# Optimization experiments

Hardware: AMD Instinct MI355X
Metric: run time of the kernel (lower is better)

Reference implementation:

```python
import jax, jax.numpy as jnp
import numpy as np

N = 50000      # nodes
E = 800000     # edges
H = 128        # hidden_features
EF = 8         # edge_features (before distance concat)
L = 2          # num_layers
NF = 100.0     # normalization_factor
NC = 1.0       # norm_constant
ATTN = True
USE_TANH = False
TANH_RANGE = 15.0
EIN = 2 * H + EF + 1  # GCL / coord-MLP edge input dim


def setup_inputs() -> dict:
    key = jax.random.key(0)
    ks = jax.random.split(key, 16)
    s = 0.02
    w = lambda k, shape: (jax.random.normal(k, shape, jnp.float32) * s)
    return dict(
        x=jax.random.normal(ks[0], (N, H), jnp.float32),
        pos=jax.random.normal(ks[1], (N, 3), jnp.float32),
        mask=jnp.ones((N, 1), jnp.float32),
        edge_attr=jax.random.normal(ks[2], (E, EF), jnp.float32),
        edge_index=jax.random.randint(ks[3], (2, E), 0, N),
        # GCL layer params, stacked over L layers
        W_e1=w(ks[4], (L, EIN, H)), b_e1=jnp.zeros((L, H), jnp.float32),
        W_e2=w(ks[5], (L, H, H)),  b_e2=jnp.zeros((L, H), jnp.float32),
        W_att=w(ks[6], (L, H, 1)), b_att=jnp.zeros((L, 1), jnp.float32),
        W_n1=w(ks[7], (L, 2 * H, H)), b_n1=jnp.zeros((L, H), jnp.float32),
        W_n2=w(ks[8], (L, H, H)),  b_n2=jnp.zeros((L, H), jnp.float32),
        # Equivariant coordinate-update MLP (last layer has no bias)
        cW1=w(ks[9], (EIN, H)), cb1=jnp.zeros((H,), jnp.float32),
        cW2=w(ks[10], (H, H)), cb2=jnp.zeros((H,), jnp.float32),
        cW3=w(ks[11], (H, 1)),
    )


def reference(x, pos, mask, edge_attr, edge_index,
              W_e1, b_e1, W_e2, b_e2, W_att, b_att, W_n1, b_n1, W_n2, b_n2,
              cW1, cb1, cW2, cb2, cW3):
    silu = jax.nn.silu
    row, col = edge_index[0], edge_index[1]  # aggregate messages at row
    diff = pos[row] - pos[col]                         # [E, 3]
    d2 = jnp.sum(diff * diff, axis=-1, keepdims=True)  # [E, 1] squared distance
    ea = jnp.concatenate([d2, edge_attr], axis=-1)     # [E, EF+1]

    # GCL message-passing layers (residual node update)
    for l in range(L):
        he = jnp.concatenate([x[row], x[col], ea], axis=-1)   # [E, EIN]
        m = silu(silu(he @ W_e1[l] + b_e1[l]) @ W_e2[l] + b_e2[l])
        if ATTN:
            m = m * jax.nn.sigmoid(m @ W_att[l] + b_att[l])
        agg = jax.ops.segment_sum(m, row, num_segments=N) / NF
        x = x + silu(jnp.concatenate([x, agg], axis=-1) @ W_n1[l] + b_n1[l]) @ W_n2[l] + b_n2[l]

    # Equivariant coordinate update
    he = jnp.concatenate([x[row], x[col], ea], axis=-1)
    phi = silu(silu(he @ cW1 + cb1) @ cW2 + cb2) @ cW3        # [E, 1]
    if USE_TANH:
        phi = jnp.tanh(phi) * TANH_RANGE
    nd = diff / (jnp.sqrt(d2) + NC)                           # normalized direction
    trans = nd * phi                                          # [E, 3]
    pos = pos + (jax.ops.segment_sum(trans, row, num_segments=N) / NF) * mask
    return (x, pos)
```

## Files before the change

kernel.cpp:

```cpp
#include <hip/hip_runtime.h>
#include <hip/hip_bf16.h>
#include <stdint.h>

#define NN 50000
#define NE 800000
#define HH 128

typedef __bf16 bf16x8 __attribute__((ext_vector_type(8)));
typedef float  f32x4  __attribute__((ext_vector_type(4)));
typedef long   f8frag;

__device__ __forceinline__ unsigned short f2bf(float f) {
  union { float f; uint32_t u; } v; v.f = f;
  uint32_t r = v.u + 0x7FFFu + ((v.u >> 16) & 1u);
  return (unsigned short)(r >> 16);
}
__device__ __forceinline__ float b2f(unsigned short u) {
  union { float f; uint32_t u; } v; v.u = (uint32_t)u << 16; return v.f;
}
#if __has_builtin(__builtin_amdgcn_cvt_pk_bf16_f32)
typedef __bf16 bf16x2 __attribute__((ext_vector_type(2)));
__device__ __forceinline__ uint32_t pack2bf(float a, float b) {
  union { bf16x2 v; uint32_t u; } t;
  t.v = __builtin_amdgcn_cvt_pk_bf16_f32(a, b);
  return t.u;
}
#else
__device__ __forceinline__ uint32_t pack2bf(float a, float b) {
  return (uint32_t)f2bf(a) | ((uint32_t)f2bf(b) << 16);
}
#endif
__device__ __forceinline__ uint8_t f2fp8(float v) {
  return (uint8_t)(__builtin_amdgcn_cvt_pk_fp8_f32(v, 0.f, 0, false) & 0xff);
}
__device__ __forceinline__ float silu_f(float x) {
  return x * __builtin_amdgcn_rcpf(1.f + __expf(-x));
}
__device__ __forceinline__ float sigm_f(float x) {
  return __builtin_amdgcn_rcpf(1.f + __expf(-x));
}

__device__ __forceinline__ bf16x8 frag_ld(const short* blk, int row, int q) {
  int c = q ^ ((row >> 1) & 3);
  return *(const bf16x8*)(blk + row * 32 + c * 8);
}
__device__ __forceinline__ int wfrag_off(int row, int q) {
  return row * 32 + ((q ^ ((row >> 1) & 3)) * 8);
}

__global__ void k_prep_weights(const float* We1, const float* We2, const float* Wn1,
                               const float* Wn2, const float* cW1, const float* cW2,
                               uint8_t* W1f8, short* W2sw, short* Wn1sw, short* Wn2sw,
                               short* W1csw) {
  int idx = blockIdx.x * 256 + threadIdx.x;
  if (idx < 110592) {
    int l = idx / 36864, rem = idx % 36864;
    const float* s = (l == 0) ? We1 : (l == 1) ? We1 + 33920 : cW1;
    int kkb = rem >> 12, r2 = rem & 4095;
    int n = r2 >> 5, kw = r2 & 31;
    int k = kkb * 32 + kw;
    float v = (k < 265) ? s[k * 128 + n] : 0.f;
    W1f8[idx] = f2fp8(v);
    return;
  }
  idx -= 110592;
  if (idx < 49152) {
    int l = idx >> 14, rem = idx & 16383;
    const float* s = (l == 0) ? We2 : (l == 1) ? We2 + 16384 : cW2;
    int kkb = rem >> 12, r2 = rem & 4095, n = r2 >> 5, kw = r2 & 31;
    int cp = kw >> 3, j = kw & 7, c = cp ^ ((n >> 1) & 3);
    int k = kkb * 32 + c * 8 + j;
    W2sw[(l << 14) + (rem)] = (short)f2bf(s[k * 128 + n]);
    return;
  }
  idx -= 49152;
  if (idx < 65536) {
    int l = idx >> 15, rem = idx & 32767;
    const float* s = Wn1 + l * 32768;
    int kkb = rem >> 12, r2 = rem & 4095, n = r2 >> 5, kw = r2 & 31;
    int cp = kw >> 3, j = kw & 7, c = cp ^ ((n >> 1) & 3);
    int k = kkb * 32 + c * 8 + j;
    Wn1sw[(l << 15) + rem] = (short)f2bf(s[k * 128 + n]);
    return;
  }
  idx -= 65536;
  if (idx < 32768) {
    int l = idx >> 14, rem = idx & 16383;
    const float* s = Wn2 + l * 16384;
    int kkb = rem >> 12, r2 = rem & 4095, n = r2 >> 5, kw = r2 & 31;
    int cp = kw >> 3, j = kw & 7, c = cp ^ ((n >> 1) & 3);
    int k = kkb * 32 + c * 8 + j;
    Wn2sw[(l << 14) + rem] = (short)f2bf(s[k * 128 + n]);
    return;
  }
  idx -= 32768;
  if (idx < 98304) {
    int l = idx / 32768, rem = idx % 32768;
    const float* s = (l == 0) ? We1 : (l == 1) ? We1 + 33920 : cW1;
    int kkb = rem >> 13, r2 = rem & 8191, n = r2 >> 5, kw = r2 & 31;
    int cp = kw >> 3, j = kw & 7, c = cp ^ ((n >> 1) & 3);
    int k = kkb * 32 + c * 8 + j;
    float v = (n < 128) ? s[k * 128 + n] : s[(128 + k) * 128 + (n - 128)];
    W1csw[l * 32768 + rem] = (short)f2bf(v);
  }
}

__global__ void k_x_prep(const float* __restrict__ x, short* __restrict__ Anode) {
  int i = blockIdx.x * 256 + threadIdx.x;
  if (i < NN * 32) {
    float4 v = ((const float4*)x)[i];
    int node = i >> 5, c4 = (i & 31) << 2;
    ushort4 pk;
    pk.x = f2bf(v.x); pk.y = f2bf(v.y); pk.z = f2bf(v.z); pk.w = f2bf(v.w);
    *(ushort4*)(Anode + node * 256 + c4) = pk;
  }
}
__global__ void k_nodeprep(const float* __restrict__ agg, short* __restrict__ Anode) {
  int i = blockIdx.x * 256 + threadIdx.x;
  if (i < NN * HH) Anode[(i >> 7) * 256 + 128 + (i & 127)] = (short)f2bf(agg[i] * 0.01f);
}
__global__ void k_edge_pre(const float* __restrict__ pos, const float* __restrict__ eattr,
                           const int* __restrict__ ei, const int* __restrict__ inv,
                           int* __restrict__ rowS, int* __restrict__ colS,
                           uint8_t* __restrict__ eaF8, float* __restrict__ ndS) {
  int e = blockIdx.x * 256 + threadIdx.x;
  if (e >= NE) return;
  int r = ei[e], c = ei[NE + e];
  float dx = pos[r * 3 + 0] - pos[c * 3 + 0];
  float dy = pos[r * 3 + 1] - pos[c * 3 + 1];
  float dz = pos[r * 3 + 2] - pos[c * 3 + 2];
  float d2 = dx * dx + dy * dy + dz * dz;
  float invd = __builtin_amdgcn_rcpf(sqrtf(d2) + 1.f);
  int p = inv[e];
  rowS[p] = r;
  colS[p] = c;
  ndS[p * 3 + 0] = dx * invd;
  ndS[p * 3 + 1] = dy * invd;
  ndS[p * 3 + 2] = dz * invd;
  const float* ea = eattr + (size_t)e * 8;
  uint32_t w0 = __builtin_amdgcn_cvt_pk_fp8_f32(d2, ea[0], 0, false);
  w0 = __builtin_amdgcn_cvt_pk_fp8_f32(ea[1], ea[2], w0, true);
  uint32_t w1 = __builtin_amdgcn_cvt_pk_fp8_f32(ea[3], ea[4], 0, false);
  w1 = __builtin_amdgcn_cvt_pk_fp8_f32(ea[5], ea[6], w1, true);
  uint32_t w2 = __builtin_amdgcn_cvt_pk_fp8_f32(ea[7], 0.f, 0, false);
  uint4 v = {w0, w1, w2, 0u};
  *(uint4*)(eaF8 + (size_t)p * 16) = v;
}
__global__ void k_pos_final(const float* __restrict__ pos, const float* __restrict__ mask,
                            const float* __restrict__ pagg, float* __restrict__ out) {
  int i = blockIdx.x * 256 + threadIdx.x;
  if (i < NN * 3) out[i] = pos[i] + pagg[i] * 0.01f * mask[i / 3];
}

__global__ void k_hist(const int* __restrict__ ei, int* __restrict__ cnt) {
  int e = blockIdx.x * 256 + threadIdx.x;
  if (e < NE) atomicAdd(&cnt[ei[e]], 1);
}
__global__ void k_scan_block(const int* __restrict__ cnt, int* __restrict__ offs,
                             int* __restrict__ bsum) {
  __shared__ int s[256];
  int i = blockIdx.x * 256 + threadIdx.x;
  int v = (i < NN) ? cnt[i] : 0;
  s[threadIdx.x] = v;
  __syncthreads();
#pragma unroll
  for (int d = 1; d < 256; d <<= 1) {
    int t = (threadIdx.x >= d) ? s[threadIdx.x - d] : 0;
    __syncthreads();
    s[threadIdx.x] += t;
    __syncthreads();
  }
  if (i < NN) offs[i] = s[threadIdx.x] - v;
  if (threadIdx.x == 255) bsum[blockIdx.x] = s[255];
}
__global__ void k_scan_top(int* __restrict__ bsum) {
  __shared__ int s[256];
  int v = (threadIdx.x < 196) ? bsum[threadIdx.x] : 0;
  s[threadIdx.x] = v;
  __syncthreads();
#pragma unroll
  for (int d = 1; d < 256; d <<= 1) {
    int t = (threadIdx.x >= d) ? s[threadIdx.x - d] : 0;
    __syncthreads();
    s[threadIdx.x] += t;
    __syncthreads();
  }
  if (threadIdx.x < 196) bsum[threadIdx.x] = s[threadIdx.x] - v;
}
__global__ void k_scan_add(int* __restrict__ offs, const int* __restrict__ bsum) {
  int i = blockIdx.x * 256 + threadIdx.x;
  if (i < NN) offs[i] += bsum[blockIdx.x];
}
__global__ void k_scatter(const int* __restrict__ ei, int* __restrict__ offs,
                          int* __restrict__ inv) {
  int e = blockIdx.x * 256 + threadIdx.x;
  if (e < NE) inv[e] = atomicAdd(&offs[ei[e]], 1);
}

__global__ __launch_bounds__(256) void k_h1(
    const short* __restrict__ Anode, const short* __restrict__ W1c,
    const float* __restrict__ b1, short* __restrict__ H1RC) {
  const int tid = threadIdx.x, lane = tid & 63, w = tid >> 6;
  const int ln = lane & 15, q = lane >> 4;
  const int tile = blockIdx.x;
  size_t nbase[4];
  int wofs[4];
#pragma unroll
  for (int i = 0; i < 4; ++i) {
    int node = tile * 64 + i * 16 + ln;
    nbase[i] = (size_t)(node < NN ? node : (NN - 1)) * 256;
    int row = w * 64 + i * 16 + ln;
    wofs[i] = row * 32 + ((q ^ ((row >> 1) & 3)) * 8);
  }
  f32x4 acc[4][4];
  const f32x4 zero4 = {0.f, 0.f, 0.f, 0.f};
#pragma unroll
  for (int mi = 0; mi < 4; ++mi)
#pragma unroll
    for (int ni = 0; ni < 4; ++ni) acc[mi][ni] = zero4;
#pragma unroll
  for (int kk = 0; kk < 4; ++kk) {
    bf16x8 af[4], bfr[4];
#pragma unroll
    for (int i = 0; i < 4; ++i) af[i] = *(const bf16x8*)(Anode + nbase[i] + kk * 32 + q * 8);
#pragma unroll
    for (int i = 0; i < 4; ++i) bfr[i] = *(const bf16x8*)(W1c + kk * 8192 + wofs[i]);
#pragma unroll
    for (int mi = 0; mi < 4; ++mi)
#pragma unroll
      for (int ni = 0; ni < 4; ++ni)
        acc[mi][ni] = __builtin_amdgcn_mfma_f32_16x16x32_bf16(af[mi], bfr[ni], acc[mi][ni], 0, 0, 0);
  }
  float b1v[4];
#pragma unroll
  for (int ni = 0; ni < 4; ++ni) {
    int ch = w * 64 + ni * 16 + ln;
    b1v[ni] = (ch < 128) ? b1[ch] : 0.f;
  }
#pragma unroll
  for (int mi = 0; mi < 4; ++mi)
#pragma unroll
    for (int r = 0; r < 4; ++r) {
      int node = tile * 64 + mi * 16 + q * 4 + r;
      if (node < NN) {
#pragma unroll
        for (int ni = 0; ni < 4; ++ni) {
          int ch = w * 64 + ni * 16 + ln;
          H1RC[(size_t)node * 256 + ch] = (short)f2bf(acc[mi][ni][r] + b1v[ni]);
        }
      }
    }
}

template <int COORD>
__global__ __launch_bounds__(256, 4) void k_edge_gemm(
    const short* __restrict__ H1RC, const uint8_t* __restrict__ eaF8,
    const int* __restrict__ rowS, const int* __restrict__ colS,
    const uint8_t* __restrict__ W1f8, const short* __restrict__ W2l,
    const float* __restrict__ b2,
    const float* __restrict__ wred, const float* __restrict__ batt,
    const float* __restrict__ ndS, float* outAcc) {
  __shared__ __align__(16) short A2s[8192];
  __shared__ float redp[64][2];
  __shared__ float redv[64];
  __shared__ int srow[64];
  __shared__ __align__(8) unsigned char srunS[64];
  __shared__ int runrowS[64];
  __shared__ int cntS[1];

  const int tid = threadIdx.x;
  const int lane = tid & 63;
  const int w = tid >> 6;
  const int ln = lane & 15, q = lane >> 4;
  const int wm = w >> 1, wn = w & 1;
  const int tile = blockIdx.x;

  if (tid < 64) srow[tid] = rowS[tile * 64 + tid];
  __syncthreads();

  bool is_start = (tid < 64) && (tid == 0 || srow[tid] != srow[tid - 1]);
  unsigned long long bmask = __ballot(is_start);
  if (tid == 0) cntS[0] = __popcll(bmask);
  if (tid < 64) {
    int run = __popcll(bmask & ((1ull << lane) - 1ull)) + (is_start ? 1 : 0) - 1;
    srunS[tid] = (unsigned char)run;
    if (is_start) runrowS[run] = srow[tid];
  }

  const int e0 = wm * 32 + ln, e1 = e0 + 16;
  const size_t hr0 = (size_t)srow[e0] * 256, hr1 = (size_t)srow[e1] * 256;
  const size_t hc0 = (size_t)colS[tile * 64 + e0] * 256 + 128;
  const size_t hc1 = (size_t)colS[tile * 64 + e1] * 256 + 128;
  const size_t ea0 = (size_t)(tile * 64 + e0) * 16 + (q & 1) * 8;
  const size_t ea1 = (size_t)(tile * 64 + e1) * 16 + (q & 1) * 8;
  int wofs8[4], wofs[4];
#pragma unroll
  for (int i = 0; i < 4; ++i) {
    wofs8[i] = (wn * 64 + i * 16 + ln) * 32 + q * 8;
    wofs[i] = wfrag_off(wn * 64 + i * 16 + ln, q);
  }

  ushort4 xr[4][2], xc[4][2];
#pragma unroll
  for (int ni = 0; ni < 4; ++ni) {
    int cb = wn * 64 + ni * 16 + q * 4;
    xr[ni][0] = *(const ushort4*)(H1RC + hr0 + cb);
    xr[ni][1] = *(const ushort4*)(H1RC + hr1 + cb);
    xc[ni][0] = *(const ushort4*)(H1RC + hc0 + cb);
    xc[ni][1] = *(const ushort4*)(H1RC + hc1 + cb);
  }

  f32x4 acc[4][2];
  const f32x4 zero4 = {0.f, 0.f, 0.f, 0.f};
#pragma unroll
  for (int ni = 0; ni < 4; ++ni)
#pragma unroll
    for (int mi = 0; mi < 2; ++mi) acc[ni][mi] = zero4;

  {
    const uint8_t* W1ea = W1f8 + 8 * 4096;
    f8frag wf[4], hf[2];
#pragma unroll
    for (int i = 0; i < 4; ++i) wf[i] = *(const f8frag*)(W1ea + wofs8[i]);
    hf[0] = (q < 2) ? *(const f8frag*)(eaF8 + ea0) : 0L;
    hf[1] = (q < 2) ? *(const f8frag*)(eaF8 + ea1) : 0L;
#pragma unroll
    for (int ni = 0; ni < 4; ++ni)
#pragma unroll
      for (int mi = 0; mi < 2; ++mi)
        acc[ni][mi] = __builtin_amdgcn_mfma_f32_16x16x32_fp8_fp8(wf[ni], hf[mi], acc[ni][mi], 0, 0, 0);
  }

#pragma unroll
  for (int ni = 0; ni < 4; ++ni) {
    int cb = wn * 64 + ni * 16 + q * 4;
    int kkb = cb >> 5, cc = (cb >> 3) & 3, j0 = cb & 7;
#pragma unroll
    for (int mi = 0; mi < 2; ++mi) {
      int edge = wm * 32 + mi * 16 + ln;
      int addr = kkb * 2048 + edge * 32 + ((cc ^ ((edge >> 1) & 3)) * 8) + j0;
      float h0 = silu_f(acc[ni][mi][0] + b2f(xr[ni][mi].x) + b2f(xc[ni][mi].x));
      float h1 = silu_f(acc[ni][mi][1] + b2f(xr[ni][mi].y) + b2f(xc[ni][mi].y));
      float h2 = silu_f(acc[ni][mi][2] + b2f(xr[ni][mi].z) + b2f(xc[ni][mi].z));
      float h3 = silu_f(acc[ni][mi][3] + b2f(xr[ni][mi].w) + b2f(xc[ni][mi].w));
      uint2 pk;
      pk.x = pack2bf(h0, h1);
      pk.y = pack2bf(h2, h3);
      *(uint2*)(A2s + addr) = pk;
    }
  }
  __syncthreads();

  f32x4 acc2[4][2];
#pragma unroll
  for (int ni = 0; ni < 4; ++ni)
#pragma unroll
    for (int mi = 0; mi < 2; ++mi) acc2[ni][mi] = zero4;
#pragma unroll
  for (int kk = 0; kk < 4; ++kk) {
    bf16x8 wf[4], hf[2];
#pragma unroll
    for (int i = 0; i < 4; ++i) wf[i] = *(const bf16x8*)(W2l + kk * 4096 + wofs[i]);
#pragma unroll
    for (int i = 0; i < 2; ++i) hf[i] = frag_ld(A2s + kk * 2048, wm * 32 + i * 16 + ln, q);
#pragma unroll
    for (int ni = 0; ni < 4; ++ni)
#pragma unroll
      for (int mi = 0; mi < 2; ++mi)
        acc2[ni][mi] = __builtin_amdgcn_mfma_f32_16x16x32_bf16(wf[ni], hf[mi], acc2[ni][mi], 0, 0, 0);
  }

  float4 b2v[4], wv[4];
#pragma unroll
  for (int ni = 0; ni < 4; ++ni) {
    b2v[ni] = *(const float4*)(b2 + wn * 64 + ni * 16 + q * 4);
    wv[ni]  = *(const float4*)(wred + wn * 64 + ni * 16 + q * 4);
  }
  float p[2] = {0.f, 0.f};
#pragma unroll
  for (int ni = 0; ni < 4; ++ni)
#pragma unroll
    for (int mi = 0; mi < 2; ++mi)
#pragma unroll
      for (int r = 0; r < 4; ++r) {
        float v = silu_f(acc2[ni][mi][r] + ((const float*)&b2v[ni])[r]);
        acc2[ni][mi][r] = v;
        p[mi] += v * ((const float*)&wv[ni])[r];
      }
#pragma unroll
  for (int mi = 0; mi < 2; ++mi) {
    p[mi] += __shfl_xor(p[mi], 16, 64);
    p[mi] += __shfl_xor(p[mi], 32, 64);
  }
  if (lane < 16) {
#pragma unroll
    for (int mi = 0; mi < 2; ++mi) redp[wm * 32 + mi * 16 + ln][wn] = p[mi];
  }
  __syncthreads();

  if (COORD == 0) {
    if (tid < 64) redv[tid] = sigm_f(redp[tid][0] + redp[tid][1] + batt[0]);
    __syncthreads();
    float attv[2] = {redv[wm * 32 + ln], redv[wm * 32 + 16 + ln]};
#pragma unroll
    for (int ni = 0; ni < 4; ++ni)
#pragma unroll
      for (int mi = 0; mi < 2; ++mi) {
        int eb = mi * 16 + ln;
        int cE = (eb >> 3) & 3, jE = eb & 7;
#pragma unroll
        for (int r = 0; r < 4; ++r) {
          int chan2 = wn * 64 + ni * 16 + q * 4 + r;
          int addr = wm * 4096 + chan2 * 32 + ((cE ^ ((chan2 >> 1) & 3)) * 8) + jE;
          union { float f; uint32_t u; } vv;
          vv.f = acc2[ni][mi][r] * attv[mi];
          A2s[addr] = (short)((vv.u + 0x8000u) >> 16);
        }
      }
    __syncthreads();
    const int nruns = cntS[0];
    bf16x8 bfrg[2][2];
#pragma unroll
    for (int kk = 0; kk < 2; ++kk)
#pragma unroll
      for (int ni = 0; ni < 2; ++ni)
        bfrg[kk][ni] = frag_ld(A2s + kk * 4096, w * 32 + ni * 16 + ln, q);
    const int npass = (nruns + 15) >> 4;
    for (int pp = 0; pp < npass; ++pp) {
      const unsigned int base = pp * 16;
      f32x4 a3c[2] = {zero4, zero4};
#pragma unroll
      for (int kk = 0; kk < 2; ++kk) {
        uint2 sb = *(const uint2*)(srunS + kk * 32 + q * 8);
        union { short s[8]; bf16x8 v; } af;
#pragma unroll
        for (int j = 0; j < 4; ++j)
          af.s[j] = (((sb.x >> (8 * j)) & 255u) == base + (unsigned)ln) ? (short)0x3F80 : (short)0;
#pragma unroll
        for (int j = 0; j < 4; ++j)
          af.s[4 + j] = (((sb.y >> (8 * j)) & 255u) == base + (unsigned)ln) ? (short)0x3F80 : (short)0;
        a3c[0] = __builtin_amdgcn_mfma_f32_16x16x32_bf16(af.v, bfrg[kk][0], a3c[0], 0, 0, 0);
        a3c[1] = __builtin_amdgcn_mfma_f32_16x16x32_bf16(af.v, bfrg[kk][1], a3c[1], 0, 0, 0);
      }
#pragma unroll
      for (int ni = 0; ni < 2; ++ni)
#pragma unroll
        for (int r = 0; r < 4; ++r) {
          int run = (int)base + q * 4 + r;
          if (run < nruns) {
            int rw = runrowS[run];
            atomicAdd(&outAcc[(size_t)rw * 128 + (w * 32 + ni * 16 + ln)], a3c[ni][r]);
          }
        }
    }
  } else {
    float* ndl = (float*)A2s;
    if (tid < 64) {
      float phi = redp[tid][0] + redp[tid][1];
      ndl[tid * 3 + 0] = ndS[(size_t)(tile * 64 + tid) * 3 + 0] * phi;
      ndl[tid * 3 + 1] = ndS[(size_t)(tile * 64 + tid) * 3 + 1] * phi;
      ndl[tid * 3 + 2] = ndS[(size_t)(tile * 64 + tid) * 3 + 2] * phi;
    }
    __syncthreads();
    if (is_start) {
      int myrow = srow[tid];
      float s0 = 0.f, s1 = 0.f, s2 = 0.f;
      for (int j = tid; j < 64 && srow[j] == myrow; ++j) {
        s0 += ndl[j * 3 + 0];
        s1 += ndl[j * 3 + 1];
        s2 += ndl[j * 3 + 2];
      }
      atomicAdd(&outAcc[myrow * 3 + 0], s0);
      atomicAdd(&outAcc[myrow * 3 + 1], s1);
      atomicAdd(&outAcc[myrow * 3 + 2], s2);
    }
  }
}

__global__ __launch_bounds__(256) void k_node_gemm(
    short* Anode, const short* __restrict__ Wn1l, const short* __restrict__ Wn2l,
    const float* __restrict__ b1, const float* __restrict__ b2,
    const float* __restrict__ xres, float* __restrict__ xout) {
  __shared__ short A2s[4 * 4096];

  const int tid = threadIdx.x;
  const int lane = tid & 63;
  const int w = tid >> 6;
  const int ln = lane & 15, q = lane >> 4;
  const int wm = w >> 1, wn = w & 1;
  const int tile = blockIdx.x;

  size_t nbase[4];
  int wofs[4];
#pragma unroll
  for (int i = 0; i < 4; ++i) {
    int node = tile * 128 + wm * 64 + i * 16 + ln;
    nbase[i] = (size_t)(node < NN ? node : (NN - 1)) * 256;
    wofs[i] = wfrag_off(wn * 64 + i * 16 + ln, q);
  }

  f32x4 acc[4][4];
  const f32x4 zero4 = {0.f, 0.f, 0.f, 0.f};
#pragma unroll
  for (int mi = 0; mi < 4; ++mi)
#pragma unroll
    for (int ni = 0; ni < 4; ++ni) acc[mi][ni] = zero4;

#pragma unroll
  for (int kk = 0; kk < 8; ++kk) {
    bf16x8 af[4], bfr[4];
#pragma unroll
    for (int i = 0; i < 4; ++i) af[i] = *(const bf16x8*)(Anode + nbase[i] + kk * 32 + q * 8);
#pragma unroll
    for (int i = 0; i < 4; ++i) bfr[i] = *(const bf16x8*)(Wn1l + kk * 4096 + wofs[i]);
#pragma unroll
    for (int mi = 0; mi < 4; ++mi)
#pragma unroll
      for (int ni = 0; ni < 4; ++ni)
        acc[mi][ni] = __builtin_amdgcn_mfma_f32_16x16x32_bf16(af[mi], bfr[ni], acc[mi][ni], 0, 0, 0);
  }

  float b1v[4];
#pragma unroll
  for (int ni = 0; ni < 4; ++ni) b1v[ni] = b1[wn * 64 + ni * 16 + ln];
#pragma unroll
  for (int mi = 0; mi < 4; ++mi)
#pragma unroll
    for (int ni = 0; ni < 4; ++ni) {
      int chan = wn * 64 + ni * 16 + ln;
      int kkb = chan >> 5, c = (chan >> 3) & 3, jj = chan & 7;
#pragma unroll
      for (int r = 0; r < 4; ++r) {
        int m = wm * 64 + mi * 16 + q * 4 + r;
        float v = silu_f(acc[mi][ni][r] + b1v[ni]);
        A2s[kkb * 4096 + m * 32 + ((c ^ ((m >> 1) & 3)) * 8) + jj] = (short)f2bf(v);
      }
    }
  __syncthreads();

  f32x4 acc2[4][4];
#pragma unroll
  for (int mi = 0; mi < 4; ++mi)
#pragma unroll
    for (int ni = 0; ni < 4; ++ni) acc2[mi][ni] = zero4;
#pragma unroll
  for (int kk = 0; kk < 4; ++kk) {
    bf16x8 af[4], bfr[4];
#pragma unroll
    for (int i = 0; i < 4; ++i) af[i] = frag_ld(A2s + kk * 4096, wm * 64 + i * 16 + ln, q);
#pragma unroll
    for (int i = 0; i < 4; ++i) bfr[i] = *(const bf16x8*)(Wn2l + kk * 4096 + wofs[i]);
#pragma unroll
    for (int mi = 0; mi < 4; ++mi)
#pragma unroll
      for (int ni = 0; ni < 4; ++ni)
        acc2[mi][ni] = __builtin_amdgcn_mfma_f32_16x16x32_bf16(af[mi], bfr[ni], acc2[mi][ni], 0, 0, 0);
  }

  float b2v[4];
#pragma unroll
  for (int ni = 0; ni < 4; ++ni) b2v[ni] = b2[wn * 64 + ni * 16 + ln];
#pragma unroll
  for (int mi = 0; mi < 4; ++mi)
#pragma unroll
    for (int r = 0; r < 4; ++r) {
      int m = wm * 64 + mi * 16 + q * 4 + r;
      int node = tile * 128 + m;
      if (node < NN) {
#pragma unroll
        for (int ni = 0; ni < 4; ++ni) {
          int chan = wn * 64 + ni * 16 + ln;
          float v = acc2[mi][ni][r] + b2v[ni] + xres[(size_t)node * 128 + chan];
          xout[(size_t)node * 128 + chan] = v;
          Anode[(size_t)node * 256 + chan] = (short)f2bf(v);
        }
      }
    }
}

extern "C" void kernel_launch(void* const* d_in, const int* in_sizes, int n_in,
                              void* d_out, int out_size, void* d_ws, size_t ws_size,
                              hipStream_t stream) {
  const float* x    = (const float*)d_in[0];
  const float* pos  = (const float*)d_in[1];
  const float* mask = (const float*)d_in[2];
  const float* eattr= (const float*)d_in[3];
  const int*   ei   = (const int*)d_in[4];
  const float* We1  = (const float*)d_in[5];
  const float* be1  = (const float*)d_in[6];
  const float* We2  = (const float*)d_in[7];
  const float* be2  = (const float*)d_in[8];
  const float* Watt = (const float*)d_in[9];
  const float* batt = (const float*)d_in[10];
  const float* Wn1  = (const float*)d_in[11];
  const float* bn1  = (const float*)d_in[12];
  const float* Wn2  = (const float*)d_in[13];
  const float* bn2  = (const float*)d_in[14];
  const float* cW1  = (const float*)d_in[15];
  const float* cb1  = (const float*)d_in[16];
  const float* cW2  = (const float*)d_in[17];
  const float* cb2  = (const float*)d_in[18];
  const float* cW3  = (const float*)d_in[19];

  char* p = (char*)d_ws;
  auto carve = [&](size_t bytes) { char* r = p; p += (bytes + 511) & ~(size_t)511; return r; };
  short*   Anode = (short*)carve((size_t)NN * 256 * 2);
  short*   H1RC  = (short*)carve((size_t)NN * 256 * 2);
  uint8_t* eaF8  = (uint8_t*)carve((size_t)NE * 16 + 256);
  int*     rowS  = (int*)carve((size_t)NE * 4);
  int*     colS  = (int*)carve((size_t)NE * 4);
  float*   ndS   = (float*)carve((size_t)NE * 3 * 4);
  float*   agg   = (float*)carve((size_t)NN * 128 * 4);
  float*   xcur  = (float*)carve((size_t)NN * 128 * 4);
  float*   pagg  = (float*)carve((size_t)NN * 3 * 4);
  uint8_t* W1f8  = (uint8_t*)carve(3 * 36864);
  short*   W2sw  = (short*)carve(3 * 16384 * 2);
  short*   Wn1sw = (short*)carve(2 * 32768 * 2);
  short*   Wn2sw = (short*)carve(2 * 16384 * 2);
  short*   W1csw = (short*)carve(3 * 32768 * 2);
  int*     cnt   = (int*)carve((size_t)NN * 4);
  int*     offs  = (int*)carve((size_t)NN * 4);
  int*     bsum  = (int*)carve(256 * 4);
  int*     inv   = (int*)carve((size_t)NE * 4);

  float* xout_f = (float*)d_out;
  float* pout_f = xout_f + NN * 128;

  k_prep_weights<<<1392, 256, 0, stream>>>(We1, We2, Wn1, Wn2, cW1, cW2,
                                           W1f8, W2sw, Wn1sw, Wn2sw, W1csw);
  k_x_prep<<<6250, 256, 0, stream>>>(x, Anode);

  hipMemsetAsync(cnt, 0, (size_t)NN * 4, stream);
  k_hist<<<3125, 256, 0, stream>>>(ei, cnt);
  k_scan_block<<<196, 256, 0, stream>>>(cnt, offs, bsum);
  k_scan_top<<<1, 256, 0, stream>>>(bsum);
  k_scan_add<<<196, 256, 0, stream>>>(offs, bsum);
  k_scatter<<<3125, 256, 0, stream>>>(ei, offs, inv);
  k_edge_pre<<<3125, 256, 0, stream>>>(pos, eattr, ei, inv, rowS, colS, eaF8, ndS);

  for (int l = 0; l < 2; ++l) {
    k_h1<<<782, 256, 0, stream>>>(Anode, W1csw + l * 32768, be1 + l * 128, H1RC);
    hipMemsetAsync(agg, 0, (size_t)NN * 128 * 4, stream);
    k_edge_gemm<0><<<12500, 256, 0, stream>>>(H1RC, eaF8, rowS, colS,
        W1f8 + l * 36864, W2sw + l * 16384, be2 + l * 128,
        Watt + l * 128, batt + l, (const float*)nullptr, agg);
    k_nodeprep<<<25000, 256, 0, stream>>>(agg, Anode);
    k_node_gemm<<<391, 256, 0, stream>>>(Anode,
        Wn1sw + l * 32768, Wn2sw + l * 16384, bn1 + l * 128, bn2 + l * 128,
        l == 0 ? x : xcur, l == 0 ? xcur : xout_f);
  }
  k_h1<<<782, 256, 0, stream>>>(Anode, W1csw + 2 * 32768, cb1, H1RC);
  hipMemsetAsync(pagg, 0, (size_t)NN * 3 * 4, stream);
  k_edge_gemm<1><<<12500, 256, 0, stream>>>(H1RC, eaF8, rowS, colS,
      W1f8 + 2 * 36864, W2sw + 2 * 16384, cb2, cW3, (const float*)nullptr, ndS, pagg);
  k_pos_final<<<587, 256, 0, stream>>>(pos, mask, pagg, pout_f);
}
```

Baseline: 799.8 us.

## Fuse agg conversion into node GEMM, permute H1RC layout, fold attention into scatter

Removes the separate k_nodeprep kernel: the node GEMM now reads fp32 agg directly, scales and packs it to bf16 in-register, and Anode shrinks to 128 channels per node. k_h1 writes H1RC in a permuted channel order so the edge GEMM can gather row/col features with two 16-byte loads per edge instead of four 8-byte loads, using 32-bit offsets. The attention sigmoid is stored as bf16 and applied as the weight in the one-hot segment-reduction MFMA, which drops a sync and a multiply per element. The node GEMM tile is halved to 64 nodes, doubling the grid size to raise occupancy.

```diff
diff --git a/kernel.cpp b/kernel.cpp
--- a/kernel.cpp
+++ b/kernel.cpp
@@ -109,15 +109,10 @@
   int i = blockIdx.x * 256 + threadIdx.x;
   if (i < NN * 32) {
     float4 v = ((const float4*)x)[i];
-    int node = i >> 5, c4 = (i & 31) << 2;
     ushort4 pk;
     pk.x = f2bf(v.x); pk.y = f2bf(v.y); pk.z = f2bf(v.z); pk.w = f2bf(v.w);
-    *(ushort4*)(Anode + node * 256 + c4) = pk;
-  }
-}
-__global__ void k_nodeprep(const float* __restrict__ agg, short* __restrict__ Anode) {
-  int i = blockIdx.x * 256 + threadIdx.x;
-  if (i < NN * HH) Anode[(i >> 7) * 256 + 128 + (i & 127)] = (short)f2bf(agg[i] * 0.01f);
+    *(ushort4*)(Anode + i * 4) = pk;
+  }
 }
 __global__ void k_edge_pre(const float* __restrict__ pos, const float* __restrict__ eattr,
                            const int* __restrict__ ei, const int* __restrict__ inv,
@@ -208,7 +203,7 @@
 #pragma unroll
   for (int i = 0; i < 4; ++i) {
     int node = tile * 64 + i * 16 + ln;
-    nbase[i] = (size_t)(node < NN ? node : (NN - 1)) * 256;
+    nbase[i] = (size_t)(node < NN ? node : (NN - 1)) * 128;
     int row = w * 64 + i * 16 + ln;
     wofs[i] = row * 32 + ((q ^ ((row >> 1) & 3)) * 8);
   }
@@ -245,8 +240,8 @@
       if (node < NN) {
 #pragma unroll
         for (int ni = 0; ni < 4; ++ni) {
-          int ch = w * 64 + ni * 16 + ln;
-          H1RC[(size_t)node * 256 + ch] = (short)f2bf(acc[mi][ni][r] + b1v[ni]);
+          int ph = (w >> 1) * 128 + (w & 1) * 64 + ((ln >> 2) << 4) + (ni << 2) + (ln & 3);
+          H1RC[(size_t)node * 256 + ph] = (short)f2bf(acc[mi][ni][r] + b1v[ni]);
         }
       }
     }
@@ -262,7 +257,7 @@
     const float* __restrict__ ndS, float* outAcc) {
   __shared__ __align__(16) short A2s[8192];
   __shared__ float redp[64][2];
-  __shared__ float redv[64];
+  __shared__ __align__(16) unsigned short attb[64];
   __shared__ int srow[64];
   __shared__ __align__(8) unsigned char srunS[64];
   __shared__ int runrowS[64];
@@ -288,11 +283,13 @@
   }
 
   const int e0 = wm * 32 + ln, e1 = e0 + 16;
-  const size_t hr0 = (size_t)srow[e0] * 256, hr1 = (size_t)srow[e1] * 256;
-  const size_t hc0 = (size_t)colS[tile * 64 + e0] * 256 + 128;
-  const size_t hc1 = (size_t)colS[tile * 64 + e1] * 256 + 128;
-  const size_t ea0 = (size_t)(tile * 64 + e0) * 16 + (q & 1) * 8;
-  const size_t ea1 = (size_t)(tile * 64 + e1) * 16 + (q & 1) * 8;
+  const uint32_t cbp = (uint32_t)(wn * 64 + q * 16);
+  const uint32_t hr0 = (uint32_t)srow[e0] * 256u + cbp;
+  const uint32_t hr1 = (uint32_t)srow[e1] * 256u + cbp;
+  const uint32_t hc0 = (uint32_t)colS[tile * 64 + e0] * 256u + 128u + cbp;
+  const uint32_t hc1 = (uint32_t)colS[tile * 64 + e1] * 256u + 128u + cbp;
+  const uint32_t ea0 = (uint32_t)(tile * 64 + e0) * 16u + (uint32_t)((q & 1) * 8);
+  const uint32_t ea1 = (uint32_t)(tile * 64 + e1) * 16u + (uint32_t)((q & 1) * 8);
   int wofs8[4], wofs[4];
 #pragma unroll
   for (int i = 0; i < 4; ++i) {
@@ -300,15 +297,16 @@
     wofs[i] = wfrag_off(wn * 64 + i * 16 + ln, q);
   }
 
-  ushort4 xr[4][2], xc[4][2];
-#pragma unroll
-  for (int ni = 0; ni < 4; ++ni) {
-    int cb = wn * 64 + ni * 16 + q * 4;
-    xr[ni][0] = *(const ushort4*)(H1RC + hr0 + cb);
-    xr[ni][1] = *(const ushort4*)(H1RC + hr1 + cb);
-    xc[ni][0] = *(const ushort4*)(H1RC + hc0 + cb);
-    xc[ni][1] = *(const ushort4*)(H1RC + hc1 + cb);
-  }
+  union U8 { uint4 v; unsigned short s[8]; };
+  U8 xr[2][2], xc[2][2];
+  xr[0][0].v = *(const uint4*)(H1RC + hr0);
+  xr[0][1].v = *(const uint4*)(H1RC + hr0 + 8);
+  xr[1][0].v = *(const uint4*)(H1RC + hr1);
+  xr[1][1].v = *(const uint4*)(H1RC + hr1 + 8);
+  xc[0][0].v = *(const uint4*)(H1RC + hc0);
+  xc[0][1].v = *(const uint4*)(H1RC + hc0 + 8);
+  xc[1][0].v = *(const uint4*)(H1RC + hc1);
+  xc[1][1].v = *(const uint4*)(H1RC + hc1 + 8);
 
   f32x4 acc[4][2];
   const f32x4 zero4 = {0.f, 0.f, 0.f, 0.f};
@@ -335,14 +333,15 @@
   for (int ni = 0; ni < 4; ++ni) {
     int cb = wn * 64 + ni * 16 + q * 4;
     int kkb = cb >> 5, cc = (cb >> 3) & 3, j0 = cb & 7;
+    const int hh = ni >> 1, b4 = (ni & 1) * 4;
 #pragma unroll
     for (int mi = 0; mi < 2; ++mi) {
       int edge = wm * 32 + mi * 16 + ln;
       int addr = kkb * 2048 + edge * 32 + ((cc ^ ((edge >> 1) & 3)) * 8) + j0;
-      float h0 = silu_f(acc[ni][mi][0] + b2f(xr[ni][mi].x) + b2f(xc[ni][mi].x));
-      float h1 = silu_f(acc[ni][mi][1] + b2f(xr[ni][mi].y) + b2f(xc[ni][mi].y));
-      float h2 = silu_f(acc[ni][mi][2] + b2f(xr[ni][mi].z) + b2f(xc[ni][mi].z));
-      float h3 = silu_f(acc[ni][mi][3] + b2f(xr[ni][mi].w) + b2f(xc[ni][mi].w));
+      float h0 = silu_f(acc[ni][mi][0] + b2f(xr[mi][hh].s[b4 + 0]) + b2f(xc[mi][hh].s[b4 + 0]));
+      float h1 = silu_f(acc[ni][mi][1] + b2f(xr[mi][hh].s[b4 + 1]) + b2f(xc[mi][hh].s[b4 + 1]));
+      float h2 = silu_f(acc[ni][mi][2] + b2f(xr[mi][hh].s[b4 + 2]) + b2f(xc[mi][hh].s[b4 + 2]));
+      float h3 = silu_f(acc[ni][mi][3] + b2f(xr[mi][hh].s[b4 + 3]) + b2f(xc[mi][hh].s[b4 + 3]));
       uint2 pk;
       pk.x = pack2bf(h0, h1);
       pk.y = pack2bf(h2, h3);
@@ -399,9 +398,7 @@
   __syncthreads();
 
   if (COORD == 0) {
-    if (tid < 64) redv[tid] = sigm_f(redp[tid][0] + redp[tid][1] + batt[0]);
-    __syncthreads();
-    float attv[2] = {redv[wm * 32 + ln], redv[wm * 32 + 16 + ln]};
+    if (tid < 64) attb[tid] = f2bf(sigm_f(redp[tid][0] + redp[tid][1] + batt[0]));
 #pragma unroll
     for (int ni = 0; ni < 4; ++ni)
 #pragma unroll
@@ -413,7 +410,7 @@
           int chan2 = wn * 64 + ni * 16 + q * 4 + r;
           int addr = wm * 4096 + chan2 * 32 + ((cE ^ ((chan2 >> 1) & 3)) * 8) + jE;
           union { float f; uint32_t u; } vv;
-          vv.f = acc2[ni][mi][r] * attv[mi];
+          vv.f = acc2[ni][mi][r];
           A2s[addr] = (short)((vv.u + 0x8000u) >> 16);
         }
       }
@@ -432,13 +429,15 @@
 #pragma unroll
       for (int kk = 0; kk < 2; ++kk) {
         uint2 sb = *(const uint2*)(srunS + kk * 32 + q * 8);
+        U8 ab;
+        ab.v = *(const uint4*)(attb + kk * 32 + q * 8);
         union { short s[8]; bf16x8 v; } af;
 #pragma unroll
         for (int j = 0; j < 4; ++j)
-          af.s[j] = (((sb.x >> (8 * j)) & 255u) == base + (unsigned)ln) ? (short)0x3F80 : (short)0;
+          af.s[j] = (((sb.x >> (8 * j)) & 255u) == base + (unsigned)ln) ? (short)ab.s[j] : (short)0;
 #pragma unroll
         for (int j = 0; j < 4; ++j)
-          af.s[4 + j] = (((sb.y >> (8 * j)) & 255u) == base + (unsigned)ln) ? (short)0x3F80 : (short)0;
+          af.s[4 + j] = (((sb.y >> (8 * j)) & 255u) == base + (unsigned)ln) ? (short)ab.s[4 + j] : (short)0;
         a3c[0] = __builtin_amdgcn_mfma_f32_16x16x32_bf16(af.v, bfrg[kk][0], a3c[0], 0, 0, 0);
         a3c[1] = __builtin_amdgcn_mfma_f32_16x16x32_bf16(af.v, bfrg[kk][1], a3c[1], 0, 0, 0);
       }
@@ -478,10 +477,11 @@
 }
 
 __global__ __launch_bounds__(256) void k_node_gemm(
-    short* Anode, const short* __restrict__ Wn1l, const short* __restrict__ Wn2l,
+    short* Anode, const float* __restrict__ agg,
+    const short* __restrict__ Wn1l, const short* __restrict__ Wn2l,
     const float* __restrict__ b1, const float* __restrict__ b2,
     const float* __restrict__ xres, float* __restrict__ xout) {
-  __shared__ short A2s[4 * 4096];
+  __shared__ short A2s[4 * 2048];
 
   const int tid = threadIdx.x;
   const int lane = tid & 63;
@@ -490,31 +490,48 @@
   const int wm = w >> 1, wn = w & 1;
   const int tile = blockIdx.x;
 
-  size_t nbase[4];
+  int nidx[2];
+  size_t nbase[2];
   int wofs[4];
 #pragma unroll
-  for (int i = 0; i < 4; ++i) {
-    int node = tile * 128 + wm * 64 + i * 16 + ln;
-    nbase[i] = (size_t)(node < NN ? node : (NN - 1)) * 256;
-    wofs[i] = wfrag_off(wn * 64 + i * 16 + ln, q);
-  }
-
-  f32x4 acc[4][4];
+  for (int i = 0; i < 2; ++i) {
+    int node = tile * 64 + wm * 32 + i * 16 + ln;
+    nidx[i] = node < NN ? node : (NN - 1);
+    nbase[i] = (size_t)nidx[i] * 128;
+  }
+#pragma unroll
+  for (int i = 0; i < 4; ++i) wofs[i] = wfrag_off(wn * 64 + i * 16 + ln, q);
+
+  f32x4 acc[2][4];
   const f32x4 zero4 = {0.f, 0.f, 0.f, 0.f};
 #pragma unroll
-  for (int mi = 0; mi < 4; ++mi)
+  for (int mi = 0; mi < 2; ++mi)
 #pragma unroll
     for (int ni = 0; ni < 4; ++ni) acc[mi][ni] = zero4;
 
 #pragma unroll
   for (int kk = 0; kk < 8; ++kk) {
-    bf16x8 af[4], bfr[4];
-#pragma unroll
-    for (int i = 0; i < 4; ++i) af[i] = *(const bf16x8*)(Anode + nbase[i] + kk * 32 + q * 8);
+    bf16x8 af[2], bfr[4];
+#pragma unroll
+    for (int i = 0; i < 2; ++i) {
+      if (kk < 4) {
+        af[i] = *(const bf16x8*)(Anode + nbase[i] + kk * 32 + q * 8);
+      } else {
+        const float* ag = agg + nbase[i] + (kk - 4) * 32 + q * 8;
+        float4 lo = *(const float4*)ag;
+        float4 hi = *(const float4*)(ag + 4);
+        union { uint32_t u[4]; bf16x8 v; } t;
+        t.u[0] = pack2bf(lo.x * 0.01f, lo.y * 0.01f);
+        t.u[1] = pack2bf(lo.z * 0.01f, lo.w * 0.01f);
+        t.u[2] = pack2bf(hi.x * 0.01f, hi.y * 0.01f);
+        t.u[3] = pack2bf(hi.z * 0.01f, hi.w * 0.01f);
+        af[i] = t.v;
+      }
+    }
 #pragma unroll
     for (int i = 0; i < 4; ++i) bfr[i] = *(const bf16x8*)(Wn1l + kk * 4096 + wofs[i]);
 #pragma unroll
-    for (int mi = 0; mi < 4; ++mi)
+    for (int mi = 0; mi < 2; ++mi)
 #pragma unroll
       for (int ni = 0; ni < 4; ++ni)
         acc[mi][ni] = __builtin_amdgcn_mfma_f32_16x16x32_bf16(af[mi], bfr[ni], acc[mi][ni], 0, 0, 0);
@@ -524,34 +541,34 @@
 #pragma unroll
   for (int ni = 0; ni < 4; ++ni) b1v[ni] = b1[wn * 64 + ni * 16 + ln];
 #pragma unroll
-  for (int mi = 0; mi < 4; ++mi)
+  for (int mi = 0; mi < 2; ++mi)
 #pragma unroll
     for (int ni = 0; ni < 4; ++ni) {
       int chan = wn * 64 + ni * 16 + ln;
       int kkb = chan >> 5, c = (chan >> 3) & 3, jj = chan & 7;
 #pragma unroll
       for (int r = 0; r < 4; ++r) {
-        int m = wm * 64 + mi * 16 + q * 4 + r;
+        int m = wm * 32 + mi * 16 + q * 4 + r;
         float v = silu_f(acc[mi][ni][r] + b1v[ni]);
-        A2s[kkb * 4096 + m * 32 + ((c ^ ((m >> 1) & 3)) * 8) + jj] = (short)f2bf(v);
+        A2s[kkb * 2048 + m * 32 + ((c ^ ((m >> 1) & 3)) * 8) + jj] = (short)f2bf(v);
       }
     }
   __syncthreads();
 
-  f32x4 acc2[4][4];
-#pragma unroll
-  for (int mi = 0; mi < 4; ++mi)
+  f32x4 acc2[2][4];
+#pragma unroll
+  for (int mi = 0; mi < 2; ++mi)
 #pragma unroll
     for (int ni = 0; ni < 4; ++ni) acc2[mi][ni] = zero4;
 #pragma unroll
   for (int kk = 0; kk < 4; ++kk) {
-    bf16x8 af[4], bfr[4];
-#pragma unroll
-    for (int i = 0; i < 4; ++i) af[i] = frag_ld(A2s + kk * 4096, wm * 64 + i * 16 + ln, q);
+    bf16x8 af[2], bfr[4];
+#pragma unroll
+    for (int i = 0; i < 2; ++i) af[i] = frag_ld(A2s + kk * 2048, wm * 32 + i * 16 + ln, q);
 #pragma unroll
     for (int i = 0; i < 4; ++i) bfr[i] = *(const bf16x8*)(Wn2l + kk * 4096 + wofs[i]);
 #pragma unroll
-    for (int mi = 0; mi < 4; ++mi)
+    for (int mi = 0; mi < 2; ++mi)
 #pragma unroll
       for (int ni = 0; ni < 4; ++ni)
         acc2[mi][ni] = __builtin_amdgcn_mfma_f32_16x16x32_bf16(af[mi], bfr[ni], acc2[mi][ni], 0, 0, 0);
@@ -561,18 +578,18 @@
 #pragma unroll
   for (int ni = 0; ni < 4; ++ni) b2v[ni] = b2[wn * 64 + ni * 16 + ln];
 #pragma unroll
-  for (int mi = 0; mi < 4; ++mi)
+  for (int mi = 0; mi < 2; ++mi)
 #pragma unroll
     for (int r = 0; r < 4; ++r) {
-      int m = wm * 64 + mi * 16 + q * 4 + r;
-      int node = tile * 128 + m;
+      int m = wm * 32 + mi * 16 + q * 4 + r;
+      int node = tile * 64 + m;
       if (node < NN) {
 #pragma unroll
         for (int ni = 0; ni < 4; ++ni) {
           int chan = wn * 64 + ni * 16 + ln;
           float v = acc2[mi][ni][r] + b2v[ni] + xres[(size_t)node * 128 + chan];
           xout[(size_t)node * 128 + chan] = v;
-          Anode[(size_t)node * 256 + chan] = (short)f2bf(v);
+          Anode[(size_t)node * 128 + chan] = (short)f2bf(v);
         }
       }
     }
@@ -604,7 +621,7 @@
 
   char* p = (char*)d_ws;
   auto carve = [&](size_t bytes) { char* r = p; p += (bytes + 511) & ~(size_t)511; return r; };
-  short*   Anode = (short*)carve((size_t)NN * 256 * 2);
+  short*   Anode = (short*)carve((size_t)NN * 128 * 2);
   short*   H1RC  = (short*)carve((size_t)NN * 256 * 2);
   uint8_t* eaF8  = (uint8_t*)carve((size_t)NE * 16 + 256);
   int*     rowS  = (int*)carve((size_t)NE * 4);
@@ -644,8 +661,7 @@
     k_edge_gemm<0><<<12500, 256, 0, stream>>>(H1RC, eaF8, rowS, colS,
         W1f8 + l * 36864, W2sw + l * 16384, be2 + l * 128,
         Watt + l * 128, batt + l, (const float*)nullptr, agg);
-    k_nodeprep<<<25000, 256, 0, stream>>>(agg, Anode);
-    k_node_gemm<<<391, 256, 0, stream>>>(Anode,
+    k_node_gemm<<<782, 256, 0, stream>>>(Anode, agg,
         Wn1sw + l * 32768, Wn2sw + l * 16384, bn1 + l * 128, bn2 + l * 128,
         l == 0 ? x : xcur, l == 0 ? xcur : xout_f);
   }
```

Result: faster. 720.5 us (-9.9%).
